# Kernel tuning notes

Hardware: AMD Instinct MI355X
Metric: run time of the kernel (lower is better)

## Reference

```python
import jax, jax.numpy as jnp
import numpy as np

VOC_QUANT = (32, 32, 32)   # voc_size = 32768
EMB_QUANT = (8, 8, 16)     # emb_size = 1024
RANKS = (1, 8, 8, 1)       # TT-ranks
PADDING_IDX = 0
EMB_SIZE = int(np.prod(EMB_QUANT))


def setup_inputs() -> dict:
    key = jax.random.key(0)
    k0, k1, k2, kx = jax.random.split(key, 4)
    x = jax.random.randint(kx, (8, 4096), 0, int(np.prod(VOC_QUANT)), dtype=jnp.int64)
    # cores stored as [voc_quant_k, r_{k-1}, emb_quant_k, r_k]
    def core(k, n, rp, e, r):
        std = (2.0 / (rp * e * r)) ** 0.5  # glorot-ish scale per core
        return jax.random.normal(k, (n, rp, e, r), dtype=jnp.float32) * std
    core0 = core(k0, VOC_QUANT[0], RANKS[0], EMB_QUANT[0], RANKS[1])
    core1 = core(k1, VOC_QUANT[1], RANKS[1], EMB_QUANT[1], RANKS[2])
    core2 = core(k2, VOC_QUANT[2], RANKS[2], EMB_QUANT[2], RANKS[3])
    return {"x": x, "core0": core0, "core1": core1, "core2": core2}


def reference(x, core0, core1, core2):
    xshape = x.shape
    flat = x.reshape(-1)                       # [N]
    N = flat.shape[0]
    # ind2sub: row-major decomposition of flat index over VOC_QUANT
    strides = (VOC_QUANT[1] * VOC_QUANT[2], VOC_QUANT[2], 1)
    idx = [(flat // s) % q for s, q in zip(strides, VOC_QUANT)]
    # gather rows from each core: g_k has shape [N, r_{k-1}, e_k, r_k]
    g0 = jnp.take(core0, idx[0], axis=0)
    g1 = jnp.take(core1, idx[1], axis=0)
    g2 = jnp.take(core2, idx[2], axis=0)
    # full(): chain of small batched contractions over the TT-ranks
    res = g0.reshape(N, EMB_QUANT[0], RANKS[1])                 # r_{-1}=1
    res = jnp.einsum('ner,nrfs->nefs', res, g1).reshape(
        N, EMB_QUANT[0] * EMB_QUANT[1], RANKS[2])
    res = jnp.einsum('ner,nrfs->nefs', res, g2).reshape(N, EMB_SIZE)  # r_d=1
    # padding mask
    res = jnp.where((flat != PADDING_IDX)[:, None], res, 0.0)
    return res.reshape(*xshape, EMB_SIZE)
```

## Files before the change

kernel.cpp:

```cpp
#include <hip/hip_runtime.h>


#define TT_A_BYTES (1024u * 512u * 2u)

typedef float f4 __attribute__((ext_vector_type(4)));

__global__ __launch_bounds__(256) void tt_precomp_kernel(
    const float* __restrict__ c0,
    const float* __restrict__ c1,
    unsigned short* __restrict__ A)
{
    __shared__ float s0[64];
    __shared__ float s1[512];
    const int i0 = blockIdx.x >> 5;
    const int i1 = blockIdx.x & 31;
    const int t  = threadIdx.x;

    if (t < 16)
        *reinterpret_cast<float4*>(s0 + t * 4) =
            *reinterpret_cast<const float4*>(c0 + i0 * 64 + t * 4);
    if (t < 128)
        *reinterpret_cast<float4*>(s1 + t * 4) =
            *reinterpret_cast<const float4*>(c1 + i1 * 512 + t * 4);
    __syncthreads();

    unsigned short* Ar = A + (size_t)blockIdx.x * 512;
    #pragma unroll
    for (int v = t; v < 512; v += 256) {
        const int pair = v >> 3;
        const int r2   = v & 7;
        const int e0   = pair >> 3;
        const int e1   = pair & 7;
        float acc = 0.f;
        #pragma unroll
        for (int r1 = 0; r1 < 8; ++r1)
            acc = fmaf(s0[e0 * 8 + r1], s1[r1 * 64 + e1 * 8 + r2], acc);
        unsigned int u = __float_as_uint(acc);
        Ar[v] = (unsigned short)((u + 0x7fffu + ((u >> 16) & 1u)) >> 16);
    }
}

template<int IPW>
__global__ __launch_bounds__(512) void tt_emb_kernel512(
    const int* __restrict__ x,
    const unsigned short* __restrict__ A,
    const float* __restrict__ c2,
    float* __restrict__ out,
    int N)
{
    __shared__ float s2[4096];
    const int t = threadIdx.x;

    #pragma unroll
    for (int i = 0; i < 2; ++i)
        *reinterpret_cast<float4*>(s2 + (i * 512 + t) * 4) =
            *reinterpret_cast<const float4*>(c2 + (i * 512 + t) * 4);
    __syncthreads();

    const int w = t >> 6;
    const int l = t & 63;
    const int prow = l >> 2;
    const int eg   = l & 3;
    const int nbase = blockIdx.x * (8 * IPW) + w * IPW;

    int flats[IPW];
    #pragma unroll
    for (int k = 0; k < IPW / 4; ++k) {
        const int4 xv = *reinterpret_cast<const int4*>(x + nbase + 4 * k);
        flats[4 * k]     = xv.x;
        flats[4 * k + 1] = xv.y;
        flats[4 * k + 2] = xv.z;
        flats[4 * k + 3] = xv.w;
    }

    uint4 abuf[3][4];
    {
        const unsigned short* Ar0 = A + (size_t)((flats[0] >> 5) & 1023) * 512;
        #pragma unroll
        for (int p = 0; p < 4; ++p)
            abuf[0][p] = *reinterpret_cast<const uint4*>(Ar0 + (prow + 16 * p) * 8);
        const unsigned short* Ar1 = A + (size_t)((flats[1] >> 5) & 1023) * 512;
        #pragma unroll
        for (int p = 0; p < 4; ++p)
            abuf[1][p] = *reinterpret_cast<const uint4*>(Ar1 + (prow + 16 * p) * 8);
    }

    #pragma unroll
    for (int g = 0; g < IPW; ++g) {
        if (g + 2 < IPW) {
            const unsigned short* Ar =
                A + (size_t)((flats[g + 2] >> 5) & 1023) * 512;
            #pragma unroll
            for (int p = 0; p < 4; ++p)
                abuf[(g + 2) % 3][p] =
                    *reinterpret_cast<const uint4*>(Ar + (prow + 16 * p) * 8);
        }

        const int flat = flats[g];
        const float* c2s = s2 + (flat & 31) * 128;
        f4 cv[8];
        #pragma unroll
        for (int r2 = 0; r2 < 8; ++r2)
            cv[r2] = *reinterpret_cast<const f4*>(c2s + r2 * 16 + eg * 4);

        f4* outp = reinterpret_cast<f4*>(out + (size_t)(nbase + g) * 1024);
        const bool pad = (flat == 0);

        #pragma unroll
        for (int p = 0; p < 4; ++p) {
            const uint4 av = abuf[g % 3][p];
            float ax[8];
            ax[0] = __uint_as_float(av.x << 16);
            ax[1] = __uint_as_float(av.x & 0xffff0000u);
            ax[2] = __uint_as_float(av.y << 16);
            ax[3] = __uint_as_float(av.y & 0xffff0000u);
            ax[4] = __uint_as_float(av.z << 16);
            ax[5] = __uint_as_float(av.z & 0xffff0000u);
            ax[6] = __uint_as_float(av.w << 16);
            ax[7] = __uint_as_float(av.w & 0xffff0000u);

            f4 o = {0.f, 0.f, 0.f, 0.f};
            #pragma unroll
            for (int r2 = 0; r2 < 8; ++r2) {
                o.x = fmaf(ax[r2], cv[r2].x, o.x);
                o.y = fmaf(ax[r2], cv[r2].y, o.y);
                o.z = fmaf(ax[r2], cv[r2].z, o.z);
                o.w = fmaf(ax[r2], cv[r2].w, o.w);
            }
            if (pad) o = (f4){0.f, 0.f, 0.f, 0.f};
            outp[l + 64 * p] = o;
        }
    }
}

template<int IPW>
__global__ __launch_bounds__(256) void tt_emb_kernel(
    const int* __restrict__ x,
    const unsigned short* __restrict__ A,
    const float* __restrict__ c2,
    float* __restrict__ out,
    int N)
{
    __shared__ float s2[4096];
    const int t = threadIdx.x;

    #pragma unroll
    for (int i = 0; i < 4; ++i)
        *reinterpret_cast<float4*>(s2 + (i * 256 + t) * 4) =
            *reinterpret_cast<const float4*>(c2 + (i * 256 + t) * 4);
    __syncthreads();

    const int w = t >> 6;
    const int l = t & 63;
    const int prow = l >> 2;
    const int eg   = l & 3;
    const int nbase = blockIdx.x * (4 * IPW) + w * IPW;

    int flats[IPW];
    #pragma unroll
    for (int k = 0; k < IPW / 4; ++k) {
        const int4 xv = *reinterpret_cast<const int4*>(x + nbase + 4 * k);
        flats[4 * k]     = xv.x;
        flats[4 * k + 1] = xv.y;
        flats[4 * k + 2] = xv.z;
        flats[4 * k + 3] = xv.w;
    }

    uint4 abuf[2][4];
    {
        const unsigned short* Ar = A + (size_t)((flats[0] >> 5) & 1023) * 512;
        #pragma unroll
        for (int p = 0; p < 4; ++p)
            abuf[0][p] = *reinterpret_cast<const uint4*>(Ar + (prow + 16 * p) * 8);
    }

    #pragma unroll
    for (int g = 0; g < IPW; ++g) {
        if (g < IPW - 1) {
            const unsigned short* Ar =
                A + (size_t)((flats[g + 1] >> 5) & 1023) * 512;
            #pragma unroll
            for (int p = 0; p < 4; ++p)
                abuf[(g + 1) & 1][p] =
                    *reinterpret_cast<const uint4*>(Ar + (prow + 16 * p) * 8);
        }

        const int flat = flats[g];
        const float* c2s = s2 + (flat & 31) * 128;
        f4 cv[8];
        #pragma unroll
        for (int r2 = 0; r2 < 8; ++r2)
            cv[r2] = *reinterpret_cast<const f4*>(c2s + r2 * 16 + eg * 4);

        f4* outp = reinterpret_cast<f4*>(out + (size_t)(nbase + g) * 1024);
        const bool pad = (flat == 0);

        #pragma unroll
        for (int p = 0; p < 4; ++p) {
            const uint4 av = abuf[g & 1][p];
            float ax[8];
            ax[0] = __uint_as_float(av.x << 16);
            ax[1] = __uint_as_float(av.x & 0xffff0000u);
            ax[2] = __uint_as_float(av.y << 16);
            ax[3] = __uint_as_float(av.y & 0xffff0000u);
            ax[4] = __uint_as_float(av.z << 16);
            ax[5] = __uint_as_float(av.z & 0xffff0000u);
            ax[6] = __uint_as_float(av.w << 16);
            ax[7] = __uint_as_float(av.w & 0xffff0000u);

            f4 o = {0.f, 0.f, 0.f, 0.f};
            #pragma unroll
            for (int r2 = 0; r2 < 8; ++r2) {
                o.x = fmaf(ax[r2], cv[r2].x, o.x);
                o.y = fmaf(ax[r2], cv[r2].y, o.y);
                o.z = fmaf(ax[r2], cv[r2].z, o.z);
                o.w = fmaf(ax[r2], cv[r2].w, o.w);
            }
            if (pad) o = (f4){0.f, 0.f, 0.f, 0.f};
            outp[l + 64 * p] = o;
        }
    }
}

__global__ __launch_bounds__(256) void tt_emb_lds_kernel(
    const int* __restrict__ x,
    const float* __restrict__ c0,
    const float* __restrict__ c1,
    const float* __restrict__ c2,
    float* __restrict__ out)
{
    const int n = blockIdx.x;
    const int t = threadIdx.x;

    __shared__ float s0[64];
    __shared__ float s1[512];
    __shared__ float s2[128];

    const int flat = x[n];
    const int i0 = (flat >> 10) & 31;
    const int i1 = (flat >> 5) & 31;
    const int i2 = flat & 31;

    if (t < 64)  s0[t] = c0[i0 * 64 + t];
    s1[t]        = c1[i1 * 512 + t];
    s1[t + 256]  = c1[i1 * 512 + 256 + t];
    if (t < 128) s2[t] = c2[i2 * 128 + t];
    __syncthreads();

    const int e0  = t >> 5;
    const int e1  = (t >> 2) & 7;
    const int e2b = (t & 3) << 2;

    float tmp[8] = {0.f, 0.f, 0.f, 0.f, 0.f, 0.f, 0.f, 0.f};
    #pragma unroll
    for (int r1 = 0; r1 < 8; ++r1) {
        const float a = s0[e0 * 8 + r1];
        #pragma unroll
        for (int r2 = 0; r2 < 8; ++r2)
            tmp[r2] = fmaf(a, s1[r1 * 64 + e1 * 8 + r2], tmp[r2]);
    }

    float res[4];
    #pragma unroll
    for (int q = 0; q < 4; ++q) {
        float acc = 0.f;
        #pragma unroll
        for (int r2 = 0; r2 < 8; ++r2)
            acc = fmaf(tmp[r2], s2[r2 * 16 + e2b + q], acc);
        res[q] = acc;
    }

    if (flat == 0) { res[0] = res[1] = res[2] = res[3] = 0.f; }

    *reinterpret_cast<float4*>(out + (size_t)n * 1024 + (size_t)t * 4) =
        make_float4(res[0], res[1], res[2], res[3]);
}

extern "C" void kernel_launch(void* const* d_in, const int* in_sizes, int n_in,
                              void* d_out, int out_size, void* d_ws, size_t ws_size,
                              hipStream_t stream) {
    const int*   x  = (const int*)d_in[0];
    const float* c0 = (const float*)d_in[1];
    const float* c1 = (const float*)d_in[2];
    const float* c2 = (const float*)d_in[3];
    float* out = (float*)d_out;

    const int N = in_sizes[0];

    if (ws_size >= TT_A_BYTES && (N % 128) == 0) {
        unsigned short* A = (unsigned short*)d_ws;
        tt_precomp_kernel<<<1024, 256, 0, stream>>>(c0, c1, A);
        tt_emb_kernel512<16><<<N / 128, 512, 0, stream>>>(x, A, c2, out, N);
    } else if (ws_size >= TT_A_BYTES && (N % 16) == 0) {
        unsigned short* A = (unsigned short*)d_ws;
        tt_precomp_kernel<<<1024, 256, 0, stream>>>(c0, c1, A);
        tt_emb_kernel<4><<<N / 16, 256, 0, stream>>>(x, A, c2, out, N);
    } else {
        tt_emb_lds_kernel<<<N, 256, 0, stream>>>(x, c0, c1, c2, out);
    }
}
```

Before: 34.77 us.

## Stage gathered bf16 A rows in LDS with coalesced loads, smaller 256-thread blocks

Measured after the change: 33.55 us. 1.04x faster.

```diff
diff --git a/kernel.cpp b/kernel.cpp
--- a/kernel.cpp
+++ b/kernel.cpp
@@ -40,28 +40,23 @@
     }
 }
 
-template<int IPW>
-__global__ __launch_bounds__(512) void tt_emb_kernel512(
+__global__ __launch_bounds__(256) void tt_emb_stage_kernel(
     const int* __restrict__ x,
     const unsigned short* __restrict__ A,
     const float* __restrict__ c2,
     float* __restrict__ out,
     int N)
 {
+    constexpr int IPW = 8;
     __shared__ float s2[4096];
+    __shared__ unsigned short sA[4 * IPW][512];
+
     const int t = threadIdx.x;
-
-    #pragma unroll
-    for (int i = 0; i < 2; ++i)
-        *reinterpret_cast<float4*>(s2 + (i * 512 + t) * 4) =
-            *reinterpret_cast<const float4*>(c2 + (i * 512 + t) * 4);
-    __syncthreads();
-
     const int w = t >> 6;
     const int l = t & 63;
     const int prow = l >> 2;
     const int eg   = l & 3;
-    const int nbase = blockIdx.x * (8 * IPW) + w * IPW;
+    const int nbase = blockIdx.x * (4 * IPW) + w * IPW;
 
     int flats[IPW];
     #pragma unroll
@@ -73,31 +68,32 @@
         flats[4 * k + 3] = xv.w;
     }
 
-    uint4 abuf[3][4];
-    {
-        const unsigned short* Ar0 = A + (size_t)((flats[0] >> 5) & 1023) * 512;
-        #pragma unroll
-        for (int p = 0; p < 4; ++p)
-            abuf[0][p] = *reinterpret_cast<const uint4*>(Ar0 + (prow + 16 * p) * 8);
-        const unsigned short* Ar1 = A + (size_t)((flats[1] >> 5) & 1023) * 512;
-        #pragma unroll
-        for (int p = 0; p < 4; ++p)
-            abuf[1][p] = *reinterpret_cast<const uint4*>(Ar1 + (prow + 16 * p) * 8);
-    }
-
+    float4 c2r[4];
+    #pragma unroll
+    for (int i = 0; i < 4; ++i)
+        c2r[i] = *reinterpret_cast<const float4*>(c2 + (i * 256 + t) * 4);
+
+    uint4 aR[IPW];
     #pragma unroll
     for (int g = 0; g < IPW; ++g) {
-        if (g + 2 < IPW) {
-            const unsigned short* Ar =
-                A + (size_t)((flats[g + 2] >> 5) & 1023) * 512;
-            #pragma unroll
-            for (int p = 0; p < 4; ++p)
-                abuf[(g + 2) % 3][p] =
-                    *reinterpret_cast<const uint4*>(Ar + (prow + 16 * p) * 8);
-        }
-
+        const unsigned short* Ar = A + (size_t)((flats[g] >> 5) & 1023) * 512;
+        aR[g] = *reinterpret_cast<const uint4*>(Ar + l * 8);
+    }
+
+    #pragma unroll
+    for (int i = 0; i < 4; ++i)
+        *reinterpret_cast<float4*>(s2 + (i * 256 + t) * 4) = c2r[i];
+    #pragma unroll
+    for (int g = 0; g < IPW; ++g)
+        reinterpret_cast<uint4*>(&sA[w * IPW + g][0])[l] = aR[g];
+    __syncthreads();
+
+    #pragma unroll
+    for (int g = 0; g < IPW; ++g) {
         const int flat = flats[g];
+        const unsigned short* As = &sA[w * IPW + g][0];
         const float* c2s = s2 + (flat & 31) * 128;
+
         f4 cv[8];
         #pragma unroll
         for (int r2 = 0; r2 < 8; ++r2)
@@ -108,7 +104,8 @@
 
         #pragma unroll
         for (int p = 0; p < 4; ++p) {
-            const uint4 av = abuf[g % 3][p];
+            const uint4 av =
+                reinterpret_cast<const uint4*>(As)[prow + 16 * p];
             float ax[8];
             ax[0] = __uint_as_float(av.x << 16);
             ax[1] = __uint_as_float(av.x & 0xffff0000u);
@@ -287,14 +284,14 @@
 
     const int N = in_sizes[0];
 
-    if (ws_size >= TT_A_BYTES && (N % 128) == 0) {
+    if (ws_size >= TT_A_BYTES && (N % 32) == 0) {
         unsigned short* A = (unsigned short*)d_ws;
         tt_precomp_kernel<<<1024, 256, 0, stream>>>(c0, c1, A);
-        tt_emb_kernel512<16><<<N / 128, 512, 0, stream>>>(x, A, c2, out, N);
-    } else if (ws_size >= TT_A_BYTES && (N % 16) == 0) {
+        tt_emb_stage_kernel<<<N / 32, 256, 0, stream>>>(x, A, c2, out, N);
+    } else if (ws_size >= TT_A_BYTES && (N % 64) == 0) {
         unsigned short* A = (unsigned short*)d_ws;
         tt_precomp_kernel<<<1024, 256, 0, stream>>>(c0, c1, A);
-        tt_emb_kernel<4><<<N / 16, 256, 0, stream>>>(x, A, c2, out, N);
+        tt_emb_kernel<16><<<N / 64, 256, 0, stream>>>(x, A, c2, out, N);
     } else {
         tt_emb_lds_kernel<<<N, 256, 0, stream>>>(x, c0, c1, c2, out);
     }
```
